# Performance work log

Measured on AMD Instinct MI355X. Metric: run time of the kernel, lower is better.

Reference implementation:

```python
import jax, jax.numpy as jnp
import numpy as np
import math

B, S, D, H, W = 4, 8192, 1024, 16, 512  # batch, seq, d_model, heads, attention_window
HD = D // H


def setup_inputs() -> dict:
    key = jax.random.key(0)
    ks = jax.random.split(key, 5)
    scale = 0.02
    return {
        "x": jax.random.normal(ks[0], (B, S, D), dtype=jnp.float32),
        "wq": jax.random.normal(ks[1], (D, D), dtype=jnp.float32) * scale,
        "bq": jnp.zeros((D,), dtype=jnp.float32),
        "wk": jax.random.normal(ks[2], (D, D), dtype=jnp.float32) * scale,
        "bk": jnp.zeros((D,), dtype=jnp.float32),
        "wv": jax.random.normal(ks[3], (D, D), dtype=jnp.float32) * scale,
        "bv": jnp.zeros((D,), dtype=jnp.float32),
        "wo": jax.random.normal(ks[4], (D, D), dtype=jnp.float32) * scale,
        "bo": jnp.zeros((D,), dtype=jnp.float32),
    }


def reference(x, wq, bq, wk, bk, wv, bv, wo, bo):
    # torch Linear: y = x @ W.T + b
    q = (x @ wq.T + bq).reshape(B, S, H, HD)
    k = (x @ wk.T + bk).reshape(B, S, H, HD)
    v = (x @ wv.T + bv).reshape(B, S, H, HD)

    nb = S // W  # number of query blocks
    qb = q.reshape(B, nb, W, H, HD)

    # pad keys/values by W at the front so every block sees a 2W key window
    kp = jnp.pad(k, ((0, 0), (W, 0), (0, 0), (0, 0)))
    vp = jnp.pad(v, ((0, 0), (W, 0), (0, 0), (0, 0)))
    # padded key indices for block n: [n*W, n*W + 2W) <-> original [n*W - W, n*W + W)
    idx = jnp.arange(nb)[:, None] * W + jnp.arange(2 * W)[None, :]  # [nb, 2W]
    kb = kp[:, idx]  # [B, nb, 2W, H, HD]
    vb = vp[:, idx]  # [B, nb, 2W, H, HD]

    scores = jnp.einsum('bnqhd,bnkhd->bnhqk', qb, kb) / math.sqrt(HD)
    valid = (idx >= W)  # padded (out-of-range) keys only occur for block 0
    scores = jnp.where(valid[None, :, None, None, :], scores, -jnp.inf)
    attn = jax.nn.softmax(scores, axis=-1)  # softmax over the block's key window

    out = jnp.einsum('bnhqk,bnkhd->bnqhd', attn, vb).reshape(B, S, D)
    return out @ wo.T + bo
```

## Files before the change

### kernel.cpp

```cpp
#include <hip/hip_runtime.h>
#include <hip/hip_bf16.h>
#include <cstdint>

typedef __bf16 bf16;
typedef __attribute__((ext_vector_type(8))) __bf16 bf16x8;
typedef __attribute__((ext_vector_type(4))) __bf16 bf16x4;
typedef __attribute__((ext_vector_type(4))) float f32x4;
typedef __attribute__((ext_vector_type(16))) float f32x16;
typedef __attribute__((ext_vector_type(4))) unsigned int u32x4;

#define B_ 4
#define S_ 8192
#define D_ 1024
#define H_ 16
#define HD_ 64
#define W_ 512
#define M_ (B_*S_)

#define EXP2F(x) __builtin_amdgcn_exp2f(x)
#define MFMA16(a,b,c) __builtin_amdgcn_mfma_f32_16x16x32_bf16(a,b,c,0,0,0)
#define MFMA32(a,b,c) __builtin_amdgcn_mfma_f32_32x32x16_bf16(a,b,c,0,0,0)

__device__ __forceinline__ void async16(const void* g, void* l) {
  __builtin_amdgcn_global_load_lds(
      (const __attribute__((address_space(1))) unsigned int*)g,
      (__attribute__((address_space(3))) unsigned int*)l, 16, 0, 0);
}

__device__ __forceinline__ void cast_region(const float* __restrict__ in,
                                            bf16* __restrict__ out, int n4,
                                            int i0, int stride) {
  for (int i = i0; i < n4; i += stride) {
    f32x4 v = ((const f32x4*)in)[i];
    bf16x4 o = { (bf16)v[0], (bf16)v[1], (bf16)v[2], (bf16)v[3] };
    ((bf16x4*)out)[i] = o;
  }
}

__global__ void cast_all(const float* __restrict__ x,  bf16* __restrict__ xb,
                         const float* __restrict__ wq, bf16* __restrict__ wqb,
                         const float* __restrict__ wk, bf16* __restrict__ wkb,
                         const float* __restrict__ wv, bf16* __restrict__ wvb,
                         const float* __restrict__ wo, bf16* __restrict__ wob) {
  int i0 = blockIdx.x * blockDim.x + threadIdx.x;
  int stride = gridDim.x * blockDim.x;
  cast_region(x,  xb,  M_*D_/4, i0, stride);
  cast_region(wq, wqb, D_*D_/4, i0, stride);
  cast_region(wk, wkb, D_*D_/4, i0, stride);
  cast_region(wv, wvb, D_*D_/4, i0, stride);
  cast_region(wo, wob, D_*D_/4, i0, stride);
}

template<int MODE>
__global__ void __launch_bounds__(256, 2) gemm_bt(
    const bf16* __restrict__ A, const bf16* __restrict__ Bw,
    const float* __restrict__ bias, void* __restrict__ outp, float scale)
{
  constexpr int K = D_, N = D_;
  __shared__ bf16 As[2][128*32];
  __shared__ bf16 Bs[2][128*32];
  int bid = blockIdx.x;
  int nid = (bid & 7) * 256 + (bid >> 3);
  int bm = nid >> 3, bn = nid & 7;
  const int tid = threadIdx.x, lane = tid & 63;
  const int w = tid >> 6, wr = w >> 1, wc = w & 1;
  f32x4 acc[4][4] = {};
  const int r0 = tid >> 2;
  const int kbyte = (tid & 3) * 16;
  const char* Ab = (const char*)(A + (size_t)bm * 128 * K);
  const char* Bb = (const char*)(Bw + (size_t)bn * 128 * K);

  auto stage = [&](int kt, int buf) {
    const size_t cb = (size_t)kt * 2 + kbyte;
    async16(Ab + (size_t)r0      * (K*2) + cb, (char*)&As[buf][0] + tid*16);
    async16(Ab + (size_t)(r0+64) * (K*2) + cb, (char*)&As[buf][0] + 4096 + tid*16);
    async16(Bb + (size_t)r0      * (K*2) + cb, (char*)&Bs[buf][0] + tid*16);
    async16(Bb + (size_t)(r0+64) * (K*2) + cb, (char*)&Bs[buf][0] + 4096 + tid*16);
  };

  stage(0, 0);
  for (int i = 0; i < 32; ++i) {
    int cur = i & 1;
    if (i < 31) {
      stage((i + 1) * 32, cur ^ 1);
      asm volatile("s_waitcnt vmcnt(4)" ::: "memory");
    } else {
      asm volatile("s_waitcnt vmcnt(0)" ::: "memory");
    }
    asm volatile("s_barrier" ::: "memory");
    bf16x8 a[4], b[4];
#pragma unroll
    for (int mi = 0; mi < 4; ++mi)
      a[mi] = *(const bf16x8*)(&As[cur][0] + (wr*64 + mi*16 + (lane & 15))*32 + ((lane >> 4)*8));
#pragma unroll
    for (int ni = 0; ni < 4; ++ni)
      b[ni] = *(const bf16x8*)(&Bs[cur][0] + (wc*64 + ni*16 + (lane & 15))*32 + ((lane >> 4)*8));
#pragma unroll
    for (int mi = 0; mi < 4; ++mi)
#pragma unroll
      for (int ni = 0; ni < 4; ++ni)
        acc[mi][ni] = MFMA16(a[mi], b[ni], acc[mi][ni]);
    asm volatile("s_barrier" ::: "memory");
  }
  int row0 = bm*128 + wr*64, col0 = bn*128 + wc*64;
  int rsub = (lane >> 4) * 4;
#pragma unroll
  for (int ni = 0; ni < 4; ++ni) {
    int col = col0 + ni*16 + (lane & 15);
    float bz = bias[col];
#pragma unroll
    for (int mi = 0; mi < 4; ++mi) {
#pragma unroll
      for (int r = 0; r < 4; ++r) {
        int row = row0 + mi*16 + rsub + r;
        float v = (acc[mi][ni][r] + bz) * scale;
        if (MODE == 0) {
          ((bf16*)outp)[(size_t)row * N + col] = (bf16)v;
        } else if (MODE == 1) {
          ((bf16*)outp)[((size_t)(row >> 13) * D_ + col) * S_ + (row & (S_-1))] = (bf16)v;
        } else {
          ((float*)outp)[(size_t)row * N + col] = v;
        }
      }
    }
  }
}

__global__ void __launch_bounds__(256, 3) attn_kernel(
    const bf16* __restrict__ Q, const bf16* __restrict__ Kb,
    const bf16* __restrict__ Vt, bf16* __restrict__ Ao)
{
  __shared__ char Klds[3][8192];
  __shared__ char Vlds[3][8192];
  int x = blockIdx.x;
  int qt = (x >> 3) & 3;
  int g  = (x & 7) + 8 * (x >> 5);
  int h = g & 15, n = (g >> 4) & 15, b = g >> 8;
  int tid = threadIdx.x, lane = tid & 63, w = tid >> 6;
  int hi = lane >> 5, qv = lane & 31;
  int qrow = n * W_ + qt * 128 + w * 32;

  const bf16* Qrow = Q + ((size_t)(b * S_ + qrow + qv)) * D_ + h * 64;
  bf16x8 Qf[4];
#pragma unroll
  for (int s = 0; s < 4; ++s) Qf[s] = *(const bf16x8*)(Qrow + s * 16 + hi * 8);

  const bf16* Kg = Kb + ((size_t)b * S_) * D_ + h * 64;
  const bf16* Vg = Vt + ((size_t)(b * H_ + h) * HD_) * S_;

  const int srow = tid >> 3;
  const int sseg = (tid & 7) ^ (srow & 7);
  const int fswq = (qv & 7) << 4;

  f32x16 O0 = {}, O1 = {};
  float m_r = -3.0e38f, l_r = 0.f;

  const int c0 = (n == 0) ? 8 : 0;
  const int ksbase = (n - 1) * W_;

  auto stage = [&](int c) {
    int ks = ksbase + c * 64;
    int so = (c % 3) * 8192;
    const bf16* kr = Kg + (size_t)(ks + srow) * D_ + sseg * 8;
    async16(kr,            &Klds[0][0] + so + tid * 16);
    async16(kr + 32 * D_,  &Klds[0][0] + so + 4096 + tid * 16);
    const bf16* vr = Vg + (size_t)srow * S_ + ks + sseg * 8;
    async16(vr,            &Vlds[0][0] + so + tid * 16);
    async16(vr + (size_t)32 * S_, &Vlds[0][0] + so + 4096 + tid * 16);
  };

  stage(c0);
  stage(c0 + 1);
  asm volatile("s_waitcnt vmcnt(4)" ::: "memory");
  asm volatile("s_barrier" ::: "memory");

  for (int c = c0; c < 16; ++c) {
    bool pre = (c + 2 < 16);
    if (pre) stage(c + 2);
    const char* kbuf = &Klds[0][0] + (c % 3) * 8192;
    const char* vbuf = &Vlds[0][0] + (c % 3) * 8192;
    f32x16 C0 = {}, C1 = {};
    __builtin_amdgcn_s_setprio(1);
#pragma unroll
    for (int s = 0; s < 4; ++s) {
      bf16x8 k0 = *(const bf16x8*)(kbuf + qv * 128        + ((s * 32 + hi * 16) ^ fswq));
      bf16x8 k1 = *(const bf16x8*)(kbuf + (32 + qv) * 128 + ((s * 32 + hi * 16) ^ fswq));
      C0 = MFMA32(k0, Qf[s], C0);
      C1 = MFMA32(k1, Qf[s], C1);
    }
    __builtin_amdgcn_s_setprio(0);
    float mx = fmaxf(C0[0], C1[0]);
#pragma unroll
    for (int r = 1; r < 16; ++r) mx = fmaxf(fmaxf(mx, C0[r]), C1[r]);
    mx = fmaxf(mx, __shfl_xor(mx, 32));
    if (!__all(mx - m_r <= 8.0f)) {
      float mn = fmaxf(m_r, mx);
      float sc = EXP2F(m_r - mn);
      m_r = mn;
      l_r *= sc;
#pragma unroll
      for (int r = 0; r < 16; ++r) { O0[r] *= sc; O1[r] *= sc; }
    }
    float ls = 0.f;
    float p0[16], p1[16];
#pragma unroll
    for (int r = 0; r < 16; ++r) {
      p0[r] = EXP2F(C0[r] - m_r);
      p1[r] = EXP2F(C1[r] - m_r);
      ls += p0[r] + p1[r];
    }
    l_r += ls;
    unsigned int L0[8], L1[8];
#pragma unroll
    for (int t = 0; t < 8; ++t) {
      asm("v_cvt_pk_bf16_f32 %0, %1, %2" : "=v"(L0[t]) : "v"(p0[2*t]), "v"(p0[2*t+1]));
      asm("v_cvt_pk_bf16_f32 %0, %1, %2" : "=v"(L1[t]) : "v"(p1[2*t]), "v"(p1[2*t+1]));
    }
    asm volatile("v_permlane32_swap_b32 %0, %1" : "+v"(L0[0]), "+v"(L0[2]));
    asm volatile("v_permlane32_swap_b32 %0, %1" : "+v"(L0[1]), "+v"(L0[3]));
    asm volatile("v_permlane32_swap_b32 %0, %1" : "+v"(L0[4]), "+v"(L0[6]));
    asm volatile("v_permlane32_swap_b32 %0, %1" : "+v"(L0[5]), "+v"(L0[7]));
    asm volatile("v_permlane32_swap_b32 %0, %1" : "+v"(L1[0]), "+v"(L1[2]));
    asm volatile("v_permlane32_swap_b32 %0, %1" : "+v"(L1[1]), "+v"(L1[3]));
    asm volatile("v_permlane32_swap_b32 %0, %1" : "+v"(L1[4]), "+v"(L1[6]));
    asm volatile("v_permlane32_swap_b32 %0, %1" : "+v"(L1[5]), "+v"(L1[7]));
    u32x4 F[2][2];
    F[0][0] = u32x4{L0[0], L0[1], L0[2], L0[3]};
    F[0][1] = u32x4{L0[4], L0[5], L0[6], L0[7]};
    F[1][0] = u32x4{L1[0], L1[1], L1[2], L1[3]};
    F[1][1] = u32x4{L1[4], L1[5], L1[6], L1[7]};
    __builtin_amdgcn_s_setprio(1);
#pragma unroll
    for (int T = 0; T < 2; ++T)
#pragma unroll
      for (int s = 0; s < 2; ++s) {
        bf16x8 pf = *(bf16x8*)&F[T][s];
        int kbyteoff = T * 64 + s * 32 + hi * 16;
        bf16x8 v0 = *(const bf16x8*)(vbuf + qv * 128        + (kbyteoff ^ fswq));
        bf16x8 v1 = *(const bf16x8*)(vbuf + (32 + qv) * 128 + (kbyteoff ^ fswq));
        O0 = MFMA32(v0, pf, O0);
        O1 = MFMA32(v1, pf, O1);
      }
    __builtin_amdgcn_s_setprio(0);
    if (pre) {
      asm volatile("s_waitcnt vmcnt(4)" ::: "memory");
    } else {
      asm volatile("s_waitcnt vmcnt(0)" ::: "memory");
    }
    asm volatile("s_barrier" ::: "memory");
  }
  float lt = l_r + __shfl_xor(l_r, 32);
  float inv = 1.0f / lt;
  size_t obase = ((size_t)(b * S_ + qrow + qv)) * D_ + h * 64;
#pragma unroll
  for (int ot = 0; ot < 2; ++ot) {
#pragma unroll
    for (int rq = 0; rq < 4; ++rq) {
      int hd = ot * 32 + 8 * rq + 4 * hi;
      bf16x4 ov;
#pragma unroll
      for (int j = 0; j < 4; ++j) {
        float val = (ot == 0 ? O0[rq*4 + j] : O1[rq*4 + j]) * inv;
        ov[j] = (bf16)val;
      }
      *(bf16x4*)(Ao + obase + hd) = ov;
    }
  }
}

extern "C" void kernel_launch(void* const* d_in, const int* in_sizes, int n_in,
                              void* d_out, int out_size, void* d_ws, size_t ws_size,
                              hipStream_t stream) {
  const float* x  = (const float*)d_in[0];
  const float* wq = (const float*)d_in[1];
  const float* bq = (const float*)d_in[2];
  const float* wk = (const float*)d_in[3];
  const float* bk = (const float*)d_in[4];
  const float* wv = (const float*)d_in[5];
  const float* bv = (const float*)d_in[6];
  const float* wo = (const float*)d_in[7];
  const float* bo = (const float*)d_in[8];
  float* out = (float*)d_out;

  char* ws = (char*)d_ws;
  const size_t sz = (size_t)M_ * D_ * 2;
  bf16* xb  = (bf16*)(ws + 0*sz);
  bf16* qb  = (bf16*)(ws + 1*sz);
  bf16* kb  = (bf16*)(ws + 2*sz);
  bf16* vt  = (bf16*)(ws + 3*sz);
  bf16* ao  = (bf16*)(ws + 4*sz);
  bf16* wqb = (bf16*)(ws + 5*sz);
  bf16* wkb = wqb + (size_t)D_*D_;
  bf16* wvb = wkb + (size_t)D_*D_;
  bf16* wob = wvb + (size_t)D_*D_;

  cast_all<<<2048, 256, 0, stream>>>(x, xb, wq, wqb, wk, wkb, wv, wvb, wo, wob);

  gemm_bt<0><<<2048, 256, 0, stream>>>(xb, wqb, bq, qb, 0.125f * 1.44269504f);
  gemm_bt<0><<<2048, 256, 0, stream>>>(xb, wkb, bk, kb, 1.0f);
  gemm_bt<1><<<2048, 256, 0, stream>>>(xb, wvb, bv, vt, 1.0f);

  attn_kernel<<<4096, 256, 0, stream>>>(qb, kb, vt, ao);

  gemm_bt<2><<<2048, 256, 0, stream>>>(ao, wob, bo, out, 1.0f);
}
```

Baseline: 563.2 us.

## Enlarge GEMM tiles to 256x256 with triple buffering and MFMA-fragment LDS layout

The projection GEMMs move from 128x128 tiles with 256 threads and double buffering to 256x256 tiles with 512 threads, 8 waves and a three-stage LDS pipeline split into half-tile loads. LDS is now written directly in MFMA fragment order, so each lane reads a contiguous 16 bytes and no swizzle is needed. The attention kernel's K/V staging gets the same fragment-ordered layout in place of XOR swizzling. The aim is to cut global traffic per FLOP and LDS address work. The cost is higher register use for the 8x4 accumulators and only 512 blocks per GEMM, which may leave CUs underused.

New measurement: 589.5 us. +4.7%, slower.

```diff
diff --git a/kernel.cpp b/kernel.cpp
--- a/kernel.cpp
+++ b/kernel.cpp
@@ -52,67 +52,87 @@
 }
 
 template<int MODE>
-__global__ void __launch_bounds__(256, 2) gemm_bt(
+__global__ void __launch_bounds__(512, 2) gemm_bt(
     const bf16* __restrict__ A, const bf16* __restrict__ Bw,
     const float* __restrict__ bias, void* __restrict__ outp, float scale)
 {
   constexpr int K = D_, N = D_;
-  __shared__ bf16 As[2][128*32];
-  __shared__ bf16 Bs[2][128*32];
+  __shared__ char lds[3 * 32768];
   int bid = blockIdx.x;
-  int nid = (bid & 7) * 256 + (bid >> 3);
-  int bm = nid >> 3, bn = nid & 7;
+  int nid = (bid & 7) * 64 + (bid >> 3);
+  int bm = nid >> 2, bn = nid & 3;
   const int tid = threadIdx.x, lane = tid & 63;
-  const int w = tid >> 6, wr = w >> 1, wc = w & 1;
-  f32x4 acc[4][4] = {};
-  const int r0 = tid >> 2;
-  const int kbyte = (tid & 3) * 16;
-  const char* Ab = (const char*)(A + (size_t)bm * 128 * K);
-  const char* Bb = (const char*)(Bw + (size_t)bn * 128 * K);
-
-  auto stage = [&](int kt, int buf) {
-    const size_t cb = (size_t)kt * 2 + kbyte;
-    async16(Ab + (size_t)r0      * (K*2) + cb, (char*)&As[buf][0] + tid*16);
-    async16(Ab + (size_t)(r0+64) * (K*2) + cb, (char*)&As[buf][0] + 4096 + tid*16);
-    async16(Bb + (size_t)r0      * (K*2) + cb, (char*)&Bs[buf][0] + tid*16);
-    async16(Bb + (size_t)(r0+64) * (K*2) + cb, (char*)&Bs[buf][0] + 4096 + tid*16);
+  const int w = tid >> 6, wr = w >> 2, wc = w & 3;
+  f32x4 acc[8][4] = {};
+  const int sR  = ((tid >> 6) * 16) + (tid & 15);
+  const int skb = ((tid >> 4) & 3) * 16;
+  const char* Ab = (const char*)(A + (size_t)bm * 256 * K);
+  const char* Bb = (const char*)(Bw + (size_t)bn * 256 * K);
+
+  auto stageA = [&](int t2, int h) {
+    char* dst = lds + (t2 % 3) * 32768 + h * 8192 + tid * 16;
+    async16(Ab + (size_t)(h * 128 + sR) * (K * 2) + t2 * 64 + skb, dst);
   };
-
-  stage(0, 0);
-  for (int i = 0; i < 32; ++i) {
-    int cur = i & 1;
-    if (i < 31) {
-      stage((i + 1) * 32, cur ^ 1);
+  auto stageB = [&](int t2, int h) {
+    char* dst = lds + (t2 % 3) * 32768 + 16384 + h * 8192 + tid * 16;
+    async16(Bb + (size_t)(h * 128 + sR) * (K * 2) + t2 * 64 + skb, dst);
+  };
+
+  stageA(0, 0); stageB(0, 0); stageA(0, 1); stageB(0, 1);
+  stageA(1, 0); stageB(1, 0); stageA(1, 1); stageB(1, 1);
+  asm volatile("s_waitcnt vmcnt(4)" ::: "memory");
+  asm volatile("s_barrier" ::: "memory");
+
+#pragma unroll 1
+  for (int t = 0; t < 32; ++t) {
+    const char* base = lds + (t % 3) * 32768;
+    const char* baseB = base + 16384;
+    bool pre = (t < 30);
+    if (pre) { stageA(t + 2, 0); stageB(t + 2, 0); }
+    bf16x8 a[4], b[4];
+#pragma unroll
+    for (int mi = 0; mi < 4; ++mi)
+      a[mi] = *(const bf16x8*)(base + (wr * 8 + mi) * 1024 + lane * 16);
+#pragma unroll
+    for (int ni = 0; ni < 4; ++ni)
+      b[ni] = *(const bf16x8*)(baseB + (wc * 4 + ni) * 1024 + lane * 16);
+    __builtin_amdgcn_s_setprio(1);
+#pragma unroll
+    for (int mi = 0; mi < 4; ++mi)
+#pragma unroll
+      for (int ni = 0; ni < 4; ++ni)
+        acc[mi][ni] = MFMA16(a[mi], b[ni], acc[mi][ni]);
+    __builtin_amdgcn_s_setprio(0);
+    if (pre) { stageA(t + 2, 1); stageB(t + 2, 1); }
+#pragma unroll
+    for (int mi = 0; mi < 4; ++mi)
+      a[mi] = *(const bf16x8*)(base + (wr * 8 + 4 + mi) * 1024 + lane * 16);
+    __builtin_amdgcn_s_setprio(1);
+#pragma unroll
+    for (int mi = 0; mi < 4; ++mi)
+#pragma unroll
+      for (int ni = 0; ni < 4; ++ni)
+        acc[4 + mi][ni] = MFMA16(a[mi], b[ni], acc[4 + mi][ni]);
+    __builtin_amdgcn_s_setprio(0);
+    if (t < 30) {
       asm volatile("s_waitcnt vmcnt(4)" ::: "memory");
     } else {
       asm volatile("s_waitcnt vmcnt(0)" ::: "memory");
     }
     asm volatile("s_barrier" ::: "memory");
-    bf16x8 a[4], b[4];
-#pragma unroll
-    for (int mi = 0; mi < 4; ++mi)
-      a[mi] = *(const bf16x8*)(&As[cur][0] + (wr*64 + mi*16 + (lane & 15))*32 + ((lane >> 4)*8));
-#pragma unroll
-    for (int ni = 0; ni < 4; ++ni)
-      b[ni] = *(const bf16x8*)(&Bs[cur][0] + (wc*64 + ni*16 + (lane & 15))*32 + ((lane >> 4)*8));
-#pragma unroll
-    for (int mi = 0; mi < 4; ++mi)
-#pragma unroll
-      for (int ni = 0; ni < 4; ++ni)
-        acc[mi][ni] = MFMA16(a[mi], b[ni], acc[mi][ni]);
-    asm volatile("s_barrier" ::: "memory");
-  }
-  int row0 = bm*128 + wr*64, col0 = bn*128 + wc*64;
+  }
+
+  int row0 = bm * 256 + wr * 128, col0 = bn * 256 + wc * 64;
   int rsub = (lane >> 4) * 4;
 #pragma unroll
   for (int ni = 0; ni < 4; ++ni) {
-    int col = col0 + ni*16 + (lane & 15);
+    int col = col0 + ni * 16 + (lane & 15);
     float bz = bias[col];
 #pragma unroll
-    for (int mi = 0; mi < 4; ++mi) {
+    for (int mi = 0; mi < 8; ++mi) {
 #pragma unroll
       for (int r = 0; r < 4; ++r) {
-        int row = row0 + mi*16 + rsub + r;
+        int row = row0 + mi * 16 + rsub + r;
         float v = (acc[mi][ni][r] + bz) * scale;
         if (MODE == 0) {
           ((bf16*)outp)[(size_t)row * N + col] = (bf16)v;
@@ -148,9 +168,8 @@
   const bf16* Kg = Kb + ((size_t)b * S_) * D_ + h * 64;
   const bf16* Vg = Vt + ((size_t)(b * H_ + h) * HD_) * S_;
 
-  const int srow = tid >> 3;
-  const int sseg = (tid & 7) ^ (srow & 7);
-  const int fswq = (qv & 7) << 4;
+  const int skey  = tid & 31;
+  const int selem = (tid >> 6) * 16 + ((tid >> 5) & 1) * 8;
 
   f32x16 O0 = {}, O1 = {};
   float m_r = -3.0e38f, l_r = 0.f;
@@ -161,12 +180,12 @@
   auto stage = [&](int c) {
     int ks = ksbase + c * 64;
     int so = (c % 3) * 8192;
-    const bf16* kr = Kg + (size_t)(ks + srow) * D_ + sseg * 8;
-    async16(kr,            &Klds[0][0] + so + tid * 16);
-    async16(kr + 32 * D_,  &Klds[0][0] + so + 4096 + tid * 16);
-    const bf16* vr = Vg + (size_t)srow * S_ + ks + sseg * 8;
-    async16(vr,            &Vlds[0][0] + so + tid * 16);
-    async16(vr + (size_t)32 * S_, &Vlds[0][0] + so + 4096 + tid * 16);
+    const bf16* kr = Kg + (size_t)(ks + skey) * D_ + selem;
+    async16(kr,                    &Klds[0][0] + so + tid * 16);
+    async16(kr + 32 * D_,          &Klds[0][0] + so + 4096 + tid * 16);
+    const bf16* vr = Vg + (size_t)skey * S_ + ks + selem;
+    async16(vr,                    &Vlds[0][0] + so + tid * 16);
+    async16(vr + (size_t)32 * S_,  &Vlds[0][0] + so + 4096 + tid * 16);
   };
 
   stage(c0);
@@ -183,8 +202,8 @@
     __builtin_amdgcn_s_setprio(1);
 #pragma unroll
     for (int s = 0; s < 4; ++s) {
-      bf16x8 k0 = *(const bf16x8*)(kbuf + qv * 128        + ((s * 32 + hi * 16) ^ fswq));
-      bf16x8 k1 = *(const bf16x8*)(kbuf + (32 + qv) * 128 + ((s * 32 + hi * 16) ^ fswq));
+      bf16x8 k0 = *(const bf16x8*)(kbuf + s * 1024 + lane * 16);
+      bf16x8 k1 = *(const bf16x8*)(kbuf + (4 + s) * 1024 + lane * 16);
       C0 = MFMA32(k0, Qf[s], C0);
       C1 = MFMA32(k1, Qf[s], C1);
     }
@@ -235,9 +254,9 @@
 #pragma unroll
       for (int s = 0; s < 2; ++s) {
         bf16x8 pf = *(bf16x8*)&F[T][s];
-        int kbyteoff = T * 64 + s * 32 + hi * 16;
-        bf16x8 v0 = *(const bf16x8*)(vbuf + qv * 128        + (kbyteoff ^ fswq));
-        bf16x8 v1 = *(const bf16x8*)(vbuf + (32 + qv) * 128 + (kbyteoff ^ fswq));
+        int ksg = T * 2 + s;
+        bf16x8 v0 = *(const bf16x8*)(vbuf + ksg * 1024 + lane * 16);
+        bf16x8 v1 = *(const bf16x8*)(vbuf + (4 + ksg) * 1024 + lane * 16);
         O0 = MFMA32(v0, pf, O0);
         O1 = MFMA32(v1, pf, O1);
       }
@@ -296,11 +315,11 @@
 
   cast_all<<<2048, 256, 0, stream>>>(x, xb, wq, wqb, wk, wkb, wv, wvb, wo, wob);
 
-  gemm_bt<0><<<2048, 256, 0, stream>>>(xb, wqb, bq, qb, 0.125f * 1.44269504f);
-  gemm_bt<0><<<2048, 256, 0, stream>>>(xb, wkb, bk, kb, 1.0f);
-  gemm_bt<1><<<2048, 256, 0, stream>>>(xb, wvb, bv, vt, 1.0f);
+  gemm_bt<0><<<512, 512, 0, stream>>>(xb, wqb, bq, qb, 0.125f * 1.44269504f);
+  gemm_bt<0><<<512, 512, 0, stream>>>(xb, wkb, bk, kb, 1.0f);
+  gemm_bt<1><<<512, 512, 0, stream>>>(xb, wvb, bv, vt, 1.0f);
 
   attn_kernel<<<4096, 256, 0, stream>>>(qb, kb, vt, ao);
 
-  gemm_bt<2><<<2048, 256, 0, stream>>>(ao, wob, bo, out, 1.0f);
-}
+  gemm_bt<2><<<512, 512, 0, stream>>>(ao, wob, bo, out, 1.0f);
+}
```
